# Kernel optimization log

Measured on AMD Instinct MI355X. Metric: run time of the kernel, lower is better.

## Reference

```python
import jax, jax.numpy as jnp
import numpy as np


def _generate_planes():
    return jnp.array([[[1, 0, 0], [0, 1, 0], [0, 0, 1]],
                      [[0, 1, 0], [0, 0, 1], [1, 0, 0]],
                      [[0, 0, 1], [1, 0, 0], [0, 1, 0]]], dtype=jnp.float32)


def _grid_sample(image, optical):
    # image: [B, C, IH, IW], optical: [B, H, W, 2] in [-1, 1]
    B, C, IH, IW = image.shape
    _, H, W, _ = optical.shape
    ix = (optical[..., 0] + 1) / 2 * (IW - 1)
    iy = (optical[..., 1] + 1) / 2 * (IH - 1)
    # corner coords are non-differentiable (torch.no_grad in original)
    ix_nw = jax.lax.stop_gradient(jnp.floor(ix))
    iy_nw = jax.lax.stop_gradient(jnp.floor(iy))
    ix_se = ix_nw + 1
    iy_se = iy_nw + 1
    # bilinear weights computed with UNclamped corners (matches original order)
    w_nw = (ix_se - ix) * (iy_se - iy)
    w_ne = (ix - ix_nw) * (iy_se - iy)
    w_sw = (ix_se - ix) * (iy - iy_nw)
    w_se = (ix - ix_nw) * (iy - iy_nw)
    # clamp indices for the gathers
    cx0 = jnp.clip(ix_nw, 0, IW - 1).astype(jnp.int32)
    cy0 = jnp.clip(iy_nw, 0, IH - 1).astype(jnp.int32)
    cx1 = jnp.clip(ix_se, 0, IW - 1).astype(jnp.int32)
    cy1 = jnp.clip(iy_se, 0, IH - 1).astype(jnp.int32)
    flat = image.reshape(B, C, IH * IW)

    def gather(cy, cx):
        idx = (cy * IW + cx).reshape(B, 1, H * W)
        v = jnp.take_along_axis(flat, jnp.broadcast_to(idx, (B, C, H * W)), axis=2)
        return v.reshape(B, C, H, W)

    out = (gather(cy0, cx0) * w_nw[:, None] + gather(cy0, cx1) * w_ne[:, None]
           + gather(cy1, cx0) * w_sw[:, None] + gather(cy1, cx1) * w_se[:, None])
    return out


def _project_onto_planes(planes, coordinates):
    # planes: [P, 3, 3]; coordinates: [N, M, 3]
    N, M, _ = coordinates.shape
    P = planes.shape[0]
    inv_planes = jnp.linalg.inv(planes)  # [P, 3, 3]
    # [N, P, M, 3] @ [P, 3, 3] -> [N, P, M, 3]
    proj = jnp.einsum('nmc,pcd->npmd', coordinates, inv_planes)
    return proj.reshape(N * P, M, 3)[..., :2]


def setup_inputs() -> dict:
    key = jax.random.key(0)
    k1, k2 = jax.random.split(key)
    N, P, C, H, W = 1, 3, 32, 256, 256
    M = 524288
    plane_features = jax.random.normal(k1, (N, P, C, H, W), dtype=jnp.float32)
    coordinates = jax.random.uniform(k2, (N, M, 3), dtype=jnp.float32, minval=-1.0, maxval=1.0)
    return {
        'plane_features': plane_features,
        'coordinates': coordinates,
        'plane_axes': _generate_planes(),
        'box_warp': 2,
    }


def reference(plane_features, coordinates, plane_axes, box_warp):
    N, P, C, H, W = plane_features.shape
    _, M, _ = coordinates.shape
    feats = plane_features.reshape(N * P, C, H, W)
    coords = (2.0 / box_warp) * coordinates
    proj = _project_onto_planes(plane_axes, coords)[:, None]  # [N*P, 1, M, 2]
    sampled = _grid_sample(feats, proj)  # [N*P, C, 1, M]
    out = jnp.transpose(sampled, (0, 3, 2, 1)).reshape(N, P, M, C)
    return out
```

## Files before the change

### kernel.cpp

```cpp
#include <hip/hip_runtime.h>

#define PP 3
#define CC 32
#define HH 256
#define WW 256
#define HWP (HH * WW)
#define NH 2
#define CH 16

typedef float     f32x4 __attribute__((ext_vector_type(4)));
typedef _Float16  f16;
typedef _Float16  f16x4 __attribute__((ext_vector_type(4)));


__global__ __launch_bounds__(256) void tp_transpose(
        const float* __restrict__ in,
        f16* __restrict__ out,
        const float* __restrict__ axes,
        const int* __restrict__ box_warp_bits,
        float* __restrict__ inv_out) {
    if (blockIdx.x == 0 && blockIdx.y == 0 && threadIdx.x < PP) {
        const int t = threadIdx.x;
        int bits = *box_warp_bits;
        float bw;
        if (bits >= 1 && bits <= 100000) bw = (float)bits;
        else                             bw = __int_as_float(bits);
        const float* a = axes + t * 9;
        float a00 = a[0], a01 = a[1], a02 = a[2];
        float a10 = a[3], a11 = a[4], a12 = a[5];
        float a20 = a[6], a21 = a[7], a22 = a[8];
        float det = a00 * (a11 * a22 - a12 * a21)
                  - a01 * (a10 * a22 - a12 * a20)
                  + a02 * (a10 * a21 - a11 * a20);
        float s = (2.0f / bw) / det;
        float* o = inv_out + t * 9;
        o[0] = (a11 * a22 - a12 * a21) * s;
        o[1] = (a02 * a21 - a01 * a22) * s;
        o[2] = (a01 * a12 - a02 * a11) * s;
        o[3] = (a12 * a20 - a10 * a22) * s;
        o[4] = (a00 * a22 - a02 * a20) * s;
        o[5] = (a02 * a10 - a00 * a12) * s;
        o[6] = (a10 * a21 - a11 * a20) * s;
        o[7] = (a01 * a20 - a00 * a21) * s;
        o[8] = (a00 * a11 - a01 * a10) * s;
    }

    __shared__ float tile[CC][33];
    const int p   = blockIdx.y;
    const int pb  = blockIdx.x * 32;
    const int tid = threadIdx.x;

    const int j     = tid & 31;
    const int cbase = tid >> 5;
    const float* ip = in + (size_t)p * CC * HWP + pb + j;
#pragma unroll
    for (int it = 0; it < 4; ++it) {
        int c = cbase + it * 8;
        tile[c][j] = __builtin_nontemporal_load(ip + (size_t)c * HWP);
    }
    __syncthreads();

    const int c4 = tid & 7;
    const int jj = tid >> 3;
    const int h  = c4 >> 2;
    const int cg = c4 & 3;
    f16x4 hv;
    hv.x = (f16)tile[c4 * 4 + 0][jj];
    hv.y = (f16)tile[c4 * 4 + 1][jj];
    hv.z = (f16)tile[c4 * 4 + 2][jj];
    hv.w = (f16)tile[c4 * 4 + 3][jj];
    f16x4* op = (f16x4*)out + ((size_t)(h * PP + p) * HWP + pb + jj) * 4 + cg;
    *op = hv;
}

__global__ __launch_bounds__(256) void tp_sample(
        const float* __restrict__ coords,
        const f16x4* __restrict__ feat_t,
        const float* __restrict__ invp,
        f32x4* __restrict__ out,
        int M) {
    const int tid = threadIdx.x;
    const int l4  = tid & 3;
    const int m   = blockIdx.x * 64 + (tid >> 2);
    const int p   = blockIdx.y;
    const int h   = blockIdx.z;
    if (m >= M) return;

    const float cx = __builtin_nontemporal_load(coords + 3 * m + 0);
    const float cy = __builtin_nontemporal_load(coords + 3 * m + 1);
    const float cz = __builtin_nontemporal_load(coords + 3 * m + 2);
    const float* iv = invp + p * 9;
    const float px = cx * iv[0] + cy * iv[3] + cz * iv[6];
    const float py = cx * iv[1] + cy * iv[4] + cz * iv[7];

    const float ix = (px + 1.0f) * 0.5f * (float)(WW - 1);
    const float iy = (py + 1.0f) * 0.5f * (float)(HH - 1);
    const float fx0 = floorf(ix), fy0 = floorf(iy);
    const float fx = ix - fx0, fy = iy - fy0;
    int x0 = (int)fx0, y0 = (int)fy0;
    int x1 = x0 + 1,   y1 = y0 + 1;
    x0 = min(max(x0, 0), WW - 1); x1 = min(max(x1, 0), WW - 1);
    y0 = min(max(y0, 0), HH - 1); y1 = min(max(y1, 0), HH - 1);
    const float w00 = (1.0f - fx) * (1.0f - fy);
    const float w01 = fx * (1.0f - fy);
    const float w10 = (1.0f - fx) * fy;
    const float w11 = fx * fy;

    const size_t base = (size_t)(h * PP + p) * HWP * 4 + l4;
    const f16x4 h00 = feat_t[base + (size_t)(y0 * WW + x0) * 4];
    const f16x4 h01 = feat_t[base + (size_t)(y0 * WW + x1) * 4];
    const f16x4 h10 = feat_t[base + (size_t)(y1 * WW + x0) * 4];
    const f16x4 h11 = feat_t[base + (size_t)(y1 * WW + x1) * 4];

    const f32x4 v00 = __builtin_convertvector(h00, f32x4);
    const f32x4 v01 = __builtin_convertvector(h01, f32x4);
    const f32x4 v10 = __builtin_convertvector(h10, f32x4);
    const f32x4 v11 = __builtin_convertvector(h11, f32x4);

    f32x4 r = v00 * w00 + v01 * w01 + v10 * w10 + v11 * w11;

    __builtin_nontemporal_store(r, &out[((size_t)p * M + m) * 8 + h * 4 + l4]);
}

extern "C" void kernel_launch(void* const* d_in, const int* in_sizes, int n_in,
                              void* d_out, int out_size, void* d_ws, size_t ws_size,
                              hipStream_t stream) {
    const float* feats  = (const float*)d_in[0];
    const float* coords = (const float*)d_in[1];
    const float* axes   = (const float*)d_in[2];
    const int*   bw     = (const int*)d_in[3];
    const int M = in_sizes[1] / 3;

    f16*   trans = (f16*)d_ws;
    float* inv   = (float*)((char*)d_ws + (size_t)NH * PP * HWP * CH * 2);

    tp_transpose<<<dim3(HWP / 32, PP), 256, 0, stream>>>(feats, trans, axes, bw, inv);
    tp_sample<<<dim3((M + 63) / 64, PP, NH), 256, 0, stream>>>(
        coords, (const f16x4*)trans, inv, (f32x4*)d_out, M);
}
```

Measured before the change: 309.4 us.

## Merge channel halves into one texel layout and batch four samples per thread

The transposed feature layout changes from two 16-channel halves to a single 32-channel fp16 texel of 64 bytes. Each sample's eight lanes now fetch one contiguous texel, and the separate grid dimension for the halves is dropped, so coordinate loads and weight math run once per sample instead of twice. Each thread also handles four samples and issues all sixteen gathers before doing any arithmetic, to raise memory-level parallelism. The cost is more registers per thread and possibly lower occupancy.

```diff
diff --git a/kernel.cpp b/kernel.cpp
--- a/kernel.cpp
+++ b/kernel.cpp
@@ -5,8 +5,7 @@
 #define HH 256
 #define WW 256
 #define HWP (HH * WW)
-#define NH 2
-#define CH 16
+#define SS 4
 
 typedef float     f32x4 __attribute__((ext_vector_type(4)));
 typedef _Float16  f16;
@@ -62,14 +61,12 @@
 
     const int c4 = tid & 7;
     const int jj = tid >> 3;
-    const int h  = c4 >> 2;
-    const int cg = c4 & 3;
     f16x4 hv;
     hv.x = (f16)tile[c4 * 4 + 0][jj];
     hv.y = (f16)tile[c4 * 4 + 1][jj];
     hv.z = (f16)tile[c4 * 4 + 2][jj];
     hv.w = (f16)tile[c4 * 4 + 3][jj];
-    f16x4* op = (f16x4*)out + ((size_t)(h * PP + p) * HWP + pb + jj) * 4 + cg;
+    f16x4* op = (f16x4*)out + ((size_t)p * HWP + pb + jj) * 8 + c4;
     *op = hv;
 }
 
@@ -80,46 +77,71 @@
         f32x4* __restrict__ out,
         int M) {
     const int tid = threadIdx.x;
-    const int l4  = tid & 3;
-    const int m   = blockIdx.x * 64 + (tid >> 2);
+    const int c4  = tid & 7;
+    const int g   = tid >> 3;
+    const int m0  = blockIdx.x * (32 * SS) + g;
     const int p   = blockIdx.y;
-    const int h   = blockIdx.z;
-    if (m >= M) return;
 
-    const float cx = __builtin_nontemporal_load(coords + 3 * m + 0);
-    const float cy = __builtin_nontemporal_load(coords + 3 * m + 1);
-    const float cz = __builtin_nontemporal_load(coords + 3 * m + 2);
     const float* iv = invp + p * 9;
-    const float px = cx * iv[0] + cy * iv[3] + cz * iv[6];
-    const float py = cx * iv[1] + cy * iv[4] + cz * iv[7];
+    const float i0 = iv[0], i1 = iv[1];
+    const float i3 = iv[3], i4 = iv[4];
+    const float i6 = iv[6], i7 = iv[7];
 
-    const float ix = (px + 1.0f) * 0.5f * (float)(WW - 1);
-    const float iy = (py + 1.0f) * 0.5f * (float)(HH - 1);
-    const float fx0 = floorf(ix), fy0 = floorf(iy);
-    const float fx = ix - fx0, fy = iy - fy0;
-    int x0 = (int)fx0, y0 = (int)fy0;
-    int x1 = x0 + 1,   y1 = y0 + 1;
-    x0 = min(max(x0, 0), WW - 1); x1 = min(max(x1, 0), WW - 1);
-    y0 = min(max(y0, 0), HH - 1); y1 = min(max(y1, 0), HH - 1);
-    const float w00 = (1.0f - fx) * (1.0f - fy);
-    const float w01 = fx * (1.0f - fy);
-    const float w10 = (1.0f - fx) * fy;
-    const float w11 = fx * fy;
+    const int bbase = p * (HWP * 8) + c4;
 
-    const size_t base = (size_t)(h * PP + p) * HWP * 4 + l4;
-    const f16x4 h00 = feat_t[base + (size_t)(y0 * WW + x0) * 4];
-    const f16x4 h01 = feat_t[base + (size_t)(y0 * WW + x1) * 4];
-    const f16x4 h10 = feat_t[base + (size_t)(y1 * WW + x0) * 4];
-    const f16x4 h11 = feat_t[base + (size_t)(y1 * WW + x1) * 4];
+    int   idx[SS][4];
+    float wgt[SS][4];
+#pragma unroll
+    for (int s = 0; s < SS; ++s) {
+        const int m  = m0 + 32 * s;
+        const int mm = (m < M) ? m : 0;
+        const float cx = __builtin_nontemporal_load(coords + 3 * mm + 0);
+        const float cy = __builtin_nontemporal_load(coords + 3 * mm + 1);
+        const float cz = __builtin_nontemporal_load(coords + 3 * mm + 2);
+        const float px = cx * i0 + cy * i3 + cz * i6;
+        const float py = cx * i1 + cy * i4 + cz * i7;
 
-    const f32x4 v00 = __builtin_convertvector(h00, f32x4);
-    const f32x4 v01 = __builtin_convertvector(h01, f32x4);
-    const f32x4 v10 = __builtin_convertvector(h10, f32x4);
-    const f32x4 v11 = __builtin_convertvector(h11, f32x4);
+        const float ix = (px + 1.0f) * 0.5f * (float)(WW - 1);
+        const float iy = (py + 1.0f) * 0.5f * (float)(HH - 1);
+        const float fx0 = floorf(ix), fy0 = floorf(iy);
+        const float fx = ix - fx0, fy = iy - fy0;
+        int x0 = (int)fx0, y0 = (int)fy0;
+        int x1 = x0 + 1,   y1 = y0 + 1;
+        x0 = min(max(x0, 0), WW - 1); x1 = min(max(x1, 0), WW - 1);
+        y0 = min(max(y0, 0), HH - 1); y1 = min(max(y1, 0), HH - 1);
+        wgt[s][0] = (1.0f - fx) * (1.0f - fy);
+        wgt[s][1] = fx * (1.0f - fy);
+        wgt[s][2] = (1.0f - fx) * fy;
+        wgt[s][3] = fx * fy;
+        idx[s][0] = (y0 * WW + x0) * 8;
+        idx[s][1] = (y0 * WW + x1) * 8;
+        idx[s][2] = (y1 * WW + x0) * 8;
+        idx[s][3] = (y1 * WW + x1) * 8;
+    }
 
-    f32x4 r = v00 * w00 + v01 * w01 + v10 * w10 + v11 * w11;
+    f16x4 hv[SS][4];
+#pragma unroll
+    for (int s = 0; s < SS; ++s) {
+#pragma unroll
+        for (int k = 0; k < 4; ++k) {
+            hv[s][k] = feat_t[bbase + idx[s][k]];
+        }
+    }
 
-    __builtin_nontemporal_store(r, &out[((size_t)p * M + m) * 8 + h * 4 + l4]);
+#pragma unroll
+    for (int s = 0; s < SS; ++s) {
+        const f32x4 v00 = __builtin_convertvector(hv[s][0], f32x4);
+        const f32x4 v01 = __builtin_convertvector(hv[s][1], f32x4);
+        const f32x4 v10 = __builtin_convertvector(hv[s][2], f32x4);
+        const f32x4 v11 = __builtin_convertvector(hv[s][3], f32x4);
+        f32x4 r = v00 * wgt[s][0] + v01 * wgt[s][1]
+                + v10 * wgt[s][2] + v11 * wgt[s][3];
+        const int m = m0 + 32 * s;
+        if (m < M) {
+            const unsigned oidx = (unsigned)(p * M + m) * 8u + c4;
+            __builtin_nontemporal_store(r, &out[oidx]);
+        }
+    }
 }
 
 extern "C" void kernel_launch(void* const* d_in, const int* in_sizes, int n_in,
@@ -132,9 +154,9 @@
     const int M = in_sizes[1] / 3;
 
     f16*   trans = (f16*)d_ws;
-    float* inv   = (float*)((char*)d_ws + (size_t)NH * PP * HWP * CH * 2);
+    float* inv   = (float*)((char*)d_ws + (size_t)PP * HWP * CC * 2);
 
     tp_transpose<<<dim3(HWP / 32, PP), 256, 0, stream>>>(feats, trans, axes, bw, inv);
-    tp_sample<<<dim3((M + 63) / 64, PP, NH), 256, 0, stream>>>(
+    tp_sample<<<dim3((M + 32 * SS - 1) / (32 * SS), PP), 256, 0, stream>>>(
         coords, (const f16x4*)trans, inv, (f32x4*)d_out, M);
 }
```

Result: faster. 271.7 us (-12.2%).
